# Optimization experiments

Measured on AMD Instinct MI355X. Metric: run time of the kernel, lower is better.

Reference implementation:

```python
import jax, jax.numpy as jnp
import numpy as np

N, D = 8192, 4096  # D must be a power of 2 for FWHT


def fwht(x):
    """Unnormalized Fast Walsh-Hadamard Transform along the last axis (len = 2^k)."""
    orig_shape = x.shape
    d = orig_shape[-1]
    x = x.reshape(-1, d)
    h = 1
    while h < d:
        x = x.reshape(-1, d // (2 * h), 2, h)
        a = x[..., 0, :]
        b = x[..., 1, :]
        x = jnp.stack([a + b, a - b], axis=-2)
        h *= 2
    return x.reshape(orig_shape)


def setup_inputs() -> dict:
    key = jax.random.key(0)
    k = jax.random.split(key, 6)
    return {
        "x": jax.random.normal(k[0], (N, D), dtype=jnp.float32),
        "s1": jax.random.normal(k[1], (D,), dtype=jnp.float32),
        "s2": jax.random.normal(k[2], (D,), dtype=jnp.float32),
        "g_mu": jax.random.normal(k[3], (D,), dtype=jnp.float32),
        "g_rho": jax.random.normal(k[4], (D,), dtype=jnpp.float32) if False else jax.random.normal(k[4], (D,), dtype=jnp.float32),
        "epsilon": jax.random.normal(k[5], (D,), dtype=jnp.float32),
    }


def reference(x, s1, s2, g_mu, g_rho, epsilon):
    # W(u) = diag(s1) H diag(u) H diag(s2); forward (sample=True):
    #   b = x @ W(g_mu).T + x @ W(softplus(g_rho) * epsilon).T
    # Per-row (H symmetric): x @ W(u).T = s1 * fwht(u * fwht(s2 * x)).
    t = fwht(x * s2)                                  # [N, D], shared between both terms
    g_noise = jax.nn.softplus(g_rho) * epsilon        # g_sigma_sqrt @ epsilon
    b = s1 * fwht(t * g_mu) + s1 * fwht(t * g_noise)  # [N, D]
    return b
```

## Files before the change

kernel.cpp:

```cpp
#include <hip/hip_runtime.h>
#include <math.h>

#define D 4096

__device__ __forceinline__ void fwht64(float* v) {
#pragma unroll
    for (int h = 1; h < 64; h <<= 1) {
#pragma unroll
        for (int i = 0; i < 64; i += 2 * h) {
#pragma unroll
            for (int j = i; j < i + h; ++j) {
                const float a = v[j];
                const float b = v[j + h];
                v[j]     = a + b;
                v[j + h] = a - b;
            }
        }
    }
}

__global__ void whvi_prep(const float* __restrict__ g_mu,
                          const float* __restrict__ g_rho,
                          const float* __restrict__ eps,
                          float* __restrict__ gq) {
    const int i = blockIdx.x * 64 + threadIdx.x;
    const int l = i >> 6, k = i & 63;
    const int e = (l & 3) | (k << 2) | ((l >> 2) << 8);
    const float r  = g_rho[e];
    const float sp = (r > 20.f) ? r : log1pf(expf(r));
    gq[i] = g_mu[e] + sp * eps[e];
}

__global__ void __launch_bounds__(64) whvi_main(
    const float* __restrict__ x,  const float* __restrict__ s1,
    const float* __restrict__ s2, const float* __restrict__ gq,
    const float* __restrict__ g_mu, const float* __restrict__ g_rho,
    const float* __restrict__ eps, float* __restrict__ out) {
    __shared__ alignas(16) float lds[D];
    const int l = threadIdx.x;
    const long long row = blockIdx.x;
    const float* xr = x + row * (long long)D;
    float v[64];

#pragma unroll
    for (int q = 0; q < 16; ++q) {
        const int base = (l << 2) + (q << 8);
        const float4 xv = *reinterpret_cast<const float4*>(xr + base);
        const float4 sv = *reinterpret_cast<const float4*>(s2 + base);
        v[4 * q + 0] = xv.x * sv.x;
        v[4 * q + 1] = xv.y * sv.y;
        v[4 * q + 2] = xv.z * sv.z;
        v[4 * q + 3] = xv.w * sv.w;
    }

    fwht64(v);

#pragma unroll
    for (int q = 0; q < 16; ++q) {
        const int addr = ((l ^ (q & 7)) << 2) + (q << 8);
        *reinterpret_cast<float4*>(&lds[addr]) =
            make_float4(v[4 * q], v[4 * q + 1], v[4 * q + 2], v[4 * q + 3]);
    }
    __syncthreads();
    {
        const int xb = (l & 3) | ((l >> 2) << 8);
        const int mk = (l >> 2) & 7;
#pragma unroll
        for (int k = 0; k < 64; ++k)
            v[k] = lds[xb + ((k ^ mk) << 2)];
    }

    fwht64(v);

    if (gq) {
#pragma unroll
        for (int m = 0; m < 16; ++m) {
            const float4 gv = *reinterpret_cast<const float4*>(gq + l * 64 + 4 * m);
            v[4 * m + 0] *= gv.x;
            v[4 * m + 1] *= gv.y;
            v[4 * m + 2] *= gv.z;
            v[4 * m + 3] *= gv.w;
        }
    } else {
#pragma unroll
        for (int k = 0; k < 64; ++k) {
            const int e = (l & 3) | (k << 2) | ((l >> 2) << 8);
            const float r  = g_rho[e];
            const float sp = (r > 20.f) ? r : log1pf(expf(r));
            v[k] *= g_mu[e] + sp * eps[e];
        }
    }

    fwht64(v);

    __syncthreads();
    {
        const int xb = (l & 3) | ((l >> 2) << 8);
        const int mk = (l >> 2) & 7;
#pragma unroll
        for (int k = 0; k < 64; ++k)
            lds[xb + ((k ^ mk) << 2)] = v[k];
    }
    __syncthreads();
#pragma unroll
    for (int q = 0; q < 16; ++q) {
        const int addr = ((l ^ (q & 7)) << 2) + (q << 8);
        const float4 t = *reinterpret_cast<const float4*>(&lds[addr]);
        v[4 * q + 0] = t.x;
        v[4 * q + 1] = t.y;
        v[4 * q + 2] = t.z;
        v[4 * q + 3] = t.w;
    }

    fwht64(v);

    float* outr = out + row * (long long)D;
#pragma unroll
    for (int q = 0; q < 16; ++q) {
        const int base = (l << 2) + (q << 8);
        const float4 sv = *reinterpret_cast<const float4*>(s1 + base);
        float4 o;
        o.x = v[4 * q + 0] * sv.x;
        o.y = v[4 * q + 1] * sv.y;
        o.z = v[4 * q + 2] * sv.z;
        o.w = v[4 * q + 3] * sv.w;
        *reinterpret_cast<float4*>(outr + base) = o;
    }
}

extern "C" void kernel_launch(void* const* d_in, const int* in_sizes, int n_in,
                              void* d_out, int out_size, void* d_ws, size_t ws_size,
                              hipStream_t stream) {
    const float* x     = (const float*)d_in[0];
    const float* s1    = (const float*)d_in[1];
    const float* s2    = (const float*)d_in[2];
    const float* g_mu  = (const float*)d_in[3];
    const float* g_rho = (const float*)d_in[4];
    const float* eps   = (const float*)d_in[5];
    float* out = (float*)d_out;
    const int rows = in_sizes[0] / D;

    float* gq = nullptr;
    if (ws_size >= (size_t)D * sizeof(float)) {
        gq = (float*)d_ws;
        whvi_prep<<<D / 64, 64, 0, stream>>>(g_mu, g_rho, eps, gq);
    }
    whvi_main<<<rows, 64, 0, stream>>>(x, s1, s2, gq, g_mu, g_rho, eps, out);
}
```

Before: 250.0 us.

## Pack four rows per block, use wave-local LDS fences, nontemporal output stores

Each 256-thread block now handles four rows, one wavefront per row, and each wave has its own LDS slice. Block-wide barriers are replaced by a wave-local lgkmcnt wait, on the assumption that a single wave's LDS traffic needs no cross-wave sync. Output writes use nontemporal stores to avoid polluting cache. The risks are correctness if wave-level LDS ordering is not guaranteed, a 64KB LDS footprint per block that can limit occupancy, and an implicit assumption that the row count is divisible by four.

```diff
diff --git a/kernel.cpp b/kernel.cpp
--- a/kernel.cpp
+++ b/kernel.cpp
@@ -2,6 +2,13 @@
 #include <math.h>
 
 #define D 4096
+#define RPB 4
+
+typedef float f4 __attribute__((ext_vector_type(4)));
+
+__device__ __forceinline__ void wave_lds_fence() {
+    __asm__ volatile("s_waitcnt lgkmcnt(0)" ::: "memory");
+}
 
 __device__ __forceinline__ void fwht64(float* v) {
 #pragma unroll
@@ -23,7 +30,7 @@
                           const float* __restrict__ g_rho,
                           const float* __restrict__ eps,
                           float* __restrict__ gq) {
-    const int i = blockIdx.x * 64 + threadIdx.x;
+    const int i = blockIdx.x * 256 + threadIdx.x;
     const int l = i >> 6, k = i & 63;
     const int e = (l & 3) | (k << 2) | ((l >> 2) << 8);
     const float r  = g_rho[e];
@@ -31,22 +38,24 @@
     gq[i] = g_mu[e] + sp * eps[e];
 }
 
-__global__ void __launch_bounds__(64) whvi_main(
+__global__ void __launch_bounds__(256) whvi_main(
     const float* __restrict__ x,  const float* __restrict__ s1,
     const float* __restrict__ s2, const float* __restrict__ gq,
     const float* __restrict__ g_mu, const float* __restrict__ g_rho,
     const float* __restrict__ eps, float* __restrict__ out) {
-    __shared__ alignas(16) float lds[D];
-    const int l = threadIdx.x;
-    const long long row = blockIdx.x;
+    __shared__ alignas(16) float lds_all[RPB][D];
+    const int l = threadIdx.x & 63;
+    const int w = threadIdx.x >> 6;
+    float* lds = lds_all[w];
+    const long long row = (long long)blockIdx.x * RPB + w;
     const float* xr = x + row * (long long)D;
     float v[64];
 
 #pragma unroll
     for (int q = 0; q < 16; ++q) {
         const int base = (l << 2) + (q << 8);
-        const float4 xv = *reinterpret_cast<const float4*>(xr + base);
-        const float4 sv = *reinterpret_cast<const float4*>(s2 + base);
+        const f4 xv = *reinterpret_cast<const f4*>(xr + base);
+        const f4 sv = *reinterpret_cast<const f4*>(s2 + base);
         v[4 * q + 0] = xv.x * sv.x;
         v[4 * q + 1] = xv.y * sv.y;
         v[4 * q + 2] = xv.z * sv.z;
@@ -58,10 +67,12 @@
 #pragma unroll
     for (int q = 0; q < 16; ++q) {
         const int addr = ((l ^ (q & 7)) << 2) + (q << 8);
-        *reinterpret_cast<float4*>(&lds[addr]) =
-            make_float4(v[4 * q], v[4 * q + 1], v[4 * q + 2], v[4 * q + 3]);
+        f4 t;
+        t.x = v[4 * q + 0]; t.y = v[4 * q + 1];
+        t.z = v[4 * q + 2]; t.w = v[4 * q + 3];
+        *reinterpret_cast<f4*>(&lds[addr]) = t;
     }
-    __syncthreads();
+    wave_lds_fence();
     {
         const int xb = (l & 3) | ((l >> 2) << 8);
         const int mk = (l >> 2) & 7;
@@ -75,7 +86,7 @@
     if (gq) {
 #pragma unroll
         for (int m = 0; m < 16; ++m) {
-            const float4 gv = *reinterpret_cast<const float4*>(gq + l * 64 + 4 * m);
+            const f4 gv = *reinterpret_cast<const f4*>(gq + l * 64 + 4 * m);
             v[4 * m + 0] *= gv.x;
             v[4 * m + 1] *= gv.y;
             v[4 * m + 2] *= gv.z;
@@ -93,7 +104,7 @@
 
     fwht64(v);
 
-    __syncthreads();
+    wave_lds_fence();
     {
         const int xb = (l & 3) | ((l >> 2) << 8);
         const int mk = (l >> 2) & 7;
@@ -101,11 +112,11 @@
         for (int k = 0; k < 64; ++k)
             lds[xb + ((k ^ mk) << 2)] = v[k];
     }
-    __syncthreads();
+    wave_lds_fence();
 #pragma unroll
     for (int q = 0; q < 16; ++q) {
         const int addr = ((l ^ (q & 7)) << 2) + (q << 8);
-        const float4 t = *reinterpret_cast<const float4*>(&lds[addr]);
+        const f4 t = *reinterpret_cast<const f4*>(&lds[addr]);
         v[4 * q + 0] = t.x;
         v[4 * q + 1] = t.y;
         v[4 * q + 2] = t.z;
@@ -118,13 +129,13 @@
 #pragma unroll
     for (int q = 0; q < 16; ++q) {
         const int base = (l << 2) + (q << 8);
-        const float4 sv = *reinterpret_cast<const float4*>(s1 + base);
-        float4 o;
+        const f4 sv = *reinterpret_cast<const f4*>(s1 + base);
+        f4 o;
         o.x = v[4 * q + 0] * sv.x;
         o.y = v[4 * q + 1] * sv.y;
         o.z = v[4 * q + 2] * sv.z;
         o.w = v[4 * q + 3] * sv.w;
-        *reinterpret_cast<float4*>(outr + base) = o;
+        __builtin_nontemporal_store(o, reinterpret_cast<f4*>(outr + base));
     }
 }
 
@@ -143,7 +154,7 @@
     float* gq = nullptr;
     if (ws_size >= (size_t)D * sizeof(float)) {
         gq = (float*)d_ws;
-        whvi_prep<<<D / 64, 64, 0, stream>>>(g_mu, g_rho, eps, gq);
+        whvi_prep<<<D / 256, 256, 0, stream>>>(g_mu, g_rho, eps, gq);
     }
-    whvi_main<<<rows, 64, 0, stream>>>(x, s1, s2, gq, g_mu, g_rho, eps, out);
+    whvi_main<<<rows / RPB, 256, 0, stream>>>(x, s1, s2, gq, g_mu, g_rho, eps, out);
 }
```

Result: slower. 261.9 us (+4.8%).
